# Kernel tuning notes

Hardware: AMD Instinct MI355X
Metric: run time of the kernel (lower is better)

Reference implementation:

```python
import jax, jax.numpy as jnp
import numpy as np

SIGMA = 5.0  # outlier threshold (LLM.int8()-style)


def setup_inputs() -> dict:
    key = jax.random.key(0)
    k1, k2 = jax.random.split(key)
    B, S, K, N = 4, 2048, 4096, 11008
    x = jax.random.normal(k1, (B, S, K), dtype=jnp.float32)
    weight = jax.random.normal(k2, (N, K), dtype=jnp.float32) * 0.02
    sigma = jnp.full((1,), SIGMA, dtype=jnp.float32)
    return {"x": x, "weight": weight, "sigma": sigma}


def reference(x, weight, sigma):
    # x: (..., K), weight: (N, K), sigma: (1,)
    N, K = weight.shape
    x2 = x.reshape(-1, K)  # (M, K)
    sig = sigma[0]

    # --- weight quantization (quant_weight, weight_only=False path) ---
    # note: torch's (1 << 8 - 1 - 1) == 1 << 6 == 64
    scale_col = jnp.max(jnp.abs(weight), axis=1) / 64.0          # (N,)
    q_weight = jnp.round(weight / scale_col[:, None])             # (N, K) int8-valued

    # --- FindOutliers: columns where any |x| > sigma ---
    col_mask = jnp.any(jnp.abs(x2) > sig, axis=0)                 # (K,) bool

    # ExtractOutliersAndSetToZeros
    x_out = jnp.where(col_mask[None, :], x2, 0.0)                 # outlier activations
    x_in = jnp.where(col_mask[None, :], 0.0, x2)                  # zeroed-out inputs

    # ExtractFP16weight: dequantized outlier weight columns; zero them in q_weight
    w_deq_out = q_weight * scale_col[:, None] * col_mask[None, :].astype(q_weight.dtype)
    q_w_in = jnp.where(col_mask[None, :], 0.0, q_weight)

    # fp16 outlier correction GEMM: (M, K) @ (K, N)
    outliers = x_out @ w_deq_out.T                                # (M, N)

    # per-row activation scale and int8 quantize
    x_scale = jnp.maximum(jnp.max(jnp.abs(x_in), axis=1) / 127.0, 1e-8)  # (M,)
    q_x = jnp.round(x_in / x_scale[:, None])                      # int8-valued

    # int8FusedDequantize: int8 GEMM + per-row/per-col dequant + outlier add
    y = (q_x @ q_w_in.T) * x_scale[:, None] * scale_col[None, :] + outliers
    return y.reshape(x.shape[:-1] + (N,))
```

## Files before the change

### kernel.cpp

```cpp
#include <hip/hip_runtime.h>
#include <hip/hip_bf16.h>
#include <stdint.h>

#define K_DIM 4096
#define BM 256
#define BN 256
#define BK 32
#define NT (K_DIM / BK)

typedef __bf16 bf16_t;
typedef __bf16 bf16x8 __attribute__((ext_vector_type(8)));
typedef __bf16 bf16x4 __attribute__((ext_vector_type(4)));
typedef float f32x4 __attribute__((ext_vector_type(4)));

__device__ inline void async16(const bf16_t* g, bf16_t* l) {
  __builtin_amdgcn_global_load_lds(
      (const __attribute__((address_space(1))) void*)g,
      (__attribute__((address_space(3))) void*)l, 16, 0, 0);
}


__device__ inline float wave_block_max(float v, float* red) {
  #pragma unroll
  for (int off = 32; off > 0; off >>= 1)
    v = fmaxf(v, __shfl_xor(v, off, 64));
  int lane = threadIdx.x & 63, wid = threadIdx.x >> 6;
  if (lane == 0) red[wid] = v;
  __syncthreads();
  return fmaxf(fmaxf(red[0], red[1]), fmaxf(red[2], red[3]));
}

__global__ __launch_bounds__(256) void colmask_kernel(
    const float* __restrict__ x, const float* __restrict__ sigma,
    int* __restrict__ mask, long total4) {
  float sig = sigma[0];
  long stride = (long)gridDim.x * blockDim.x;
  for (long i = (long)blockIdx.x * blockDim.x + threadIdx.x; i < total4;
       i += stride) {
    float4 v = ((const float4*)x)[i];
    int k = (int)((i * 4) & (K_DIM - 1));
    if (fabsf(v.x) > sig) mask[k + 0] = 1;
    if (fabsf(v.y) > sig) mask[k + 1] = 1;
    if (fabsf(v.z) > sig) mask[k + 2] = 1;
    if (fabsf(v.w) > sig) mask[k + 3] = 1;
  }
}

__global__ __launch_bounds__(256) void fused_w_kernel(
    const float* __restrict__ W, float* __restrict__ scale,
    bf16_t* __restrict__ Wq) {
  __shared__ float red[4];
  int n = blockIdx.x;
  const float4* row = (const float4*)(W + (size_t)n * K_DIM);
  float4 v[4];
  float amax = 0.f;
  #pragma unroll
  for (int j = 0; j < 4; j++) {
    v[j] = row[threadIdx.x + j * 256];
    amax = fmaxf(amax, fmaxf(fmaxf(fabsf(v[j].x), fabsf(v[j].y)),
                             fmaxf(fabsf(v[j].z), fabsf(v[j].w))));
  }
  float mx = wave_block_max(amax, red);
  float s = mx * (1.0f / 64.0f);
  if (threadIdx.x == 0) scale[n] = s;
  float is = (s > 0.f) ? 1.0f / s : 0.f;
  bf16_t* orow = Wq + (size_t)n * K_DIM;
  #pragma unroll
  for (int j = 0; j < 4; j++) {
    bf16x4 q;
    q[0] = (bf16_t)rintf(v[j].x * is);
    q[1] = (bf16_t)rintf(v[j].y * is);
    q[2] = (bf16_t)rintf(v[j].z * is);
    q[3] = (bf16_t)rintf(v[j].w * is);
    *(bf16x4*)(orow + (size_t)(threadIdx.x + j * 256) * 4) = q;
  }
}

__global__ __launch_bounds__(256) void fused_x_kernel(
    const float* __restrict__ x, const int* __restrict__ mask,
    float* __restrict__ xs, bf16_t* __restrict__ Aq) {
  __shared__ float red[4];
  int m = blockIdx.x;
  const float4* row = (const float4*)(x + (size_t)m * K_DIM);
  const int4* mk = (const int4*)mask;
  float4 v[4];
  int4 b[4];
  float amax = 0.f;
  #pragma unroll
  for (int j = 0; j < 4; j++) {
    v[j] = row[threadIdx.x + j * 256];
    b[j] = mk[threadIdx.x + j * 256];
    if (!b[j].x) amax = fmaxf(amax, fabsf(v[j].x));
    if (!b[j].y) amax = fmaxf(amax, fabsf(v[j].y));
    if (!b[j].z) amax = fmaxf(amax, fabsf(v[j].z));
    if (!b[j].w) amax = fmaxf(amax, fabsf(v[j].w));
  }
  float mx = wave_block_max(amax, red);
  float s = fmaxf(mx * (1.0f / 127.0f), 1e-8f);
  if (threadIdx.x == 0) xs[m] = s;
  float iv = 1.0f / s;
  bf16_t* orow = Aq + (size_t)m * K_DIM;
  #pragma unroll
  for (int j = 0; j < 4; j++) {
    float f0 = v[j].x * iv, f1 = v[j].y * iv, f2 = v[j].z * iv, f3 = v[j].w * iv;
    bf16x4 q;
    q[0] = (bf16_t)(b[j].x ? f0 : rintf(f0));
    q[1] = (bf16_t)(b[j].y ? f1 : rintf(f1));
    q[2] = (bf16_t)(b[j].z ? f2 : rintf(f2));
    q[3] = (bf16_t)(b[j].w ? f3 : rintf(f3));
    *(bf16x4*)(orow + (size_t)(threadIdx.x + j * 256) * 4) = q;
  }
}


__global__ __launch_bounds__(512, 2) void gemm_kernel(
    const bf16_t* __restrict__ A, const bf16_t* __restrict__ B,
    const float* __restrict__ xs, const float* __restrict__ sc,
    float* __restrict__ out, int M, int N) {
  __shared__ __align__(16) bf16_t lds[4 * 16384];

  const int tid  = threadIdx.x;
  const int lane = tid & 63;
  const int wave = tid >> 6;
  const int wmBase = (wave >> 2) * 128;
  const int wnBase = (wave & 3) * 64;
  const int l15  = lane & 15;
  const int quad = lane >> 4;
  const int swz8 = (quad ^ ((l15 >> 1) & 3)) * 8;

  const int ntn = N / BN;
  const int nwg = (M / BM) * ntn;
  int bid = blockIdx.x;
  int lid = (bid & 7) * (nwg >> 3) + (bid >> 3);
  const int g4 = ntn * 4;
  const int tm = (lid / g4) * 4 + (lid & 3);
  const int tn = (lid % g4) >> 2;
  const int bm = tm * BM;
  const int bn = tn * BN;

  const int srow = wave * 16 + (lane >> 2);
  const int scol = ((lane & 3) ^ ((lane >> 3) & 3)) * 8;
  const bf16_t* gA = A + (size_t)(bm + srow) * K_DIM + scol;
  const bf16_t* gB = B + (size_t)(bn + srow) * K_DIM + scol;
  bf16_t* ldsA = lds + wave * 512;
  bf16_t* ldsB = lds + 8192 + wave * 512;

  auto stageA = [&](int t) {
    const bf16_t* g = gA + (size_t)t * BK;
    bf16_t* d = ldsA + (t & 3) * 16384;
    async16(g, d);
    async16(g + (size_t)128 * K_DIM, d + 4096);
  };
  auto stageB = [&](int t) {
    const bf16_t* g = gB + (size_t)t * BK;
    bf16_t* d = ldsB + (t & 3) * 16384;
    async16(g, d);
    async16(g + (size_t)128 * K_DIM, d + 4096);
  };

  f32x4 acc[8][4];
  #pragma unroll
  for (int i = 0; i < 8; ++i)
    #pragma unroll
    for (int j = 0; j < 4; ++j)
      #pragma unroll
      for (int e = 0; e < 4; ++e) acc[i][j][e] = 0.f;

  stageA(0); stageB(0); stageA(1); stageB(1); stageA(2); stageB(2);
  asm volatile("s_waitcnt vmcnt(8)" ::: "memory");
  __builtin_amdgcn_s_barrier();

  for (int t = 0; t < NT; ++t) {
    const bf16_t* Asl = lds + (t & 3) * 16384;
    const bf16_t* Bsl = Asl + 8192;
    bf16x8 afA[4], bfr[4], afB[4];

    #pragma unroll
    for (int i = 0; i < 4; ++i)
      afA[i] = *(const bf16x8*)(Asl + (wmBase + i * 16 + l15) * 32 + swz8);
    #pragma unroll
    for (int j = 0; j < 4; ++j)
      bfr[j] = *(const bf16x8*)(Bsl + (wnBase + j * 16 + l15) * 32 + swz8);
    #pragma unroll
    for (int i = 0; i < 4; ++i)
      afB[i] = *(const bf16x8*)(Asl + (wmBase + 64 + i * 16 + l15) * 32 + swz8);

    if (t + 3 < NT) { stageA(t + 3); stageB(t + 3); }
    __builtin_amdgcn_sched_barrier(0);

    __builtin_amdgcn_s_setprio(1);
    #pragma unroll
    for (int i = 0; i < 4; ++i)
      #pragma unroll
      for (int j = 0; j < 4; ++j)
        acc[i][j] = __builtin_amdgcn_mfma_f32_16x16x32_bf16(afA[i], bfr[j],
                                                            acc[i][j], 0, 0, 0);
    __builtin_amdgcn_s_setprio(0);
    __builtin_amdgcn_sched_barrier(0);

    __builtin_amdgcn_s_setprio(1);
    #pragma unroll
    for (int i = 0; i < 4; ++i)
      #pragma unroll
      for (int j = 0; j < 4; ++j)
        acc[4 + i][j] = __builtin_amdgcn_mfma_f32_16x16x32_bf16(afB[i], bfr[j],
                                                                acc[4 + i][j], 0, 0, 0);
    __builtin_amdgcn_s_setprio(0);
    __builtin_amdgcn_sched_barrier(0);

    if (t + 1 < NT) {
      int rem = NT - 1 - t;
      if (rem >= 3)      asm volatile("s_waitcnt vmcnt(8)" ::: "memory");
      else if (rem == 2) asm volatile("s_waitcnt vmcnt(4)" ::: "memory");
      else               asm volatile("s_waitcnt vmcnt(0)" ::: "memory");
      __builtin_amdgcn_s_barrier();
    }
  }

  float scv[4];
  #pragma unroll
  for (int tj = 0; tj < 4; ++tj) scv[tj] = sc[bn + wnBase + tj * 16 + l15];
  #pragma unroll
  for (int mi = 0; mi < 8; ++mi) {
    #pragma unroll
    for (int i = 0; i < 4; ++i) {
      int row = bm + wmBase + mi * 16 + quad * 4 + i;
      float s_row = xs[row];
      float* orow = out + (size_t)row * N + bn + wnBase + l15;
      #pragma unroll
      for (int tj = 0; tj < 4; ++tj)
        orow[tj * 16] = acc[mi][tj][i] * s_row * scv[tj];
    }
  }
}


extern "C" void kernel_launch(void* const* d_in, const int* in_sizes, int n_in,
                              void* d_out, int out_size, void* d_ws, size_t ws_size,
                              hipStream_t stream) {
  const float* x = (const float*)d_in[0];
  const float* W = (const float*)d_in[1];
  const float* sigma = (const float*)d_in[2];
  float* out = (float*)d_out;

  const int K = K_DIM;
  const int M = in_sizes[0] / K;
  const int N = in_sizes[1] / K;

  char* ws = (char*)d_ws;
  size_t off = 0;
  auto alloc = [&](size_t bytes) -> void* {
    void* p = ws + off;
    off += (bytes + 255) & ~(size_t)255;
    return p;
  };
  float* scale_col = (float*)alloc((size_t)N * 4);
  int*   mask      = (int*)alloc((size_t)K * 4);
  float* xs        = (float*)alloc((size_t)M * 4);
  bf16_t* Wq       = (bf16_t*)alloc((size_t)N * K * 2);
  bf16_t* Aq       = (bf16_t*)alloc((size_t)M * K * 2);

  hipMemsetAsync(mask, 0, (size_t)K * sizeof(int), stream);

  long total4 = (long)M * K / 4;
  colmask_kernel<<<4096, 256, 0, stream>>>(x, sigma, mask, total4);

  fused_w_kernel<<<N, 256, 0, stream>>>(W, scale_col, Wq);
  fused_x_kernel<<<M, 256, 0, stream>>>(x, mask, xs, Aq);

  dim3 grid((M / BM) * (N / BN));
  gemm_kernel<<<grid, 512, 0, stream>>>(Aq, Wq, xs, scale_col, out, M, N);
}
```

Measured before the change: 1.202 ms.

## Software-pipeline LDS fragment loads with ping-pong registers and split global staging

Restructures the bf16 GEMM main loop so that each K-tile's second half of MFMAs overlaps with LDS reads of the next tile's A/B fragments. Ping-pong register sets alternate between tiles, and the A and B global-to-LDS async copies are issued in separate halves, with finer waitcnt and barrier placement. This is meant to hide LDS read latency and spread memory issue across the MFMA stream, at the cost of more registers (extra fragment sets) and more complex synchronization. The last four tiles keep a simpler epilogue loop.

```diff
diff --git a/kernel.cpp b/kernel.cpp
--- a/kernel.cpp
+++ b/kernel.cpp
@@ -166,56 +166,112 @@
       #pragma unroll
       for (int e = 0; e < 4; ++e) acc[i][j][e] = 0.f;
 
+  bf16x8 afA_p[4], bfr_p[4], afA_q[4], bfr_q[4], afB[4];
+
   stageA(0); stageB(0); stageA(1); stageB(1); stageA(2); stageB(2);
   asm volatile("s_waitcnt vmcnt(8)" ::: "memory");
   __builtin_amdgcn_s_barrier();
-
-  for (int t = 0; t < NT; ++t) {
-    const bf16_t* Asl = lds + (t & 3) * 16384;
+  {
+    const bf16_t* Asl = lds;
+    const bf16_t* Bsl = lds + 8192;
+    #pragma unroll
+    for (int i = 0; i < 4; ++i)
+      afA_p[i] = *(const bf16x8*)(Asl + (wmBase + i * 16 + l15) * 32 + swz8);
+    #pragma unroll
+    for (int j = 0; j < 4; ++j)
+      bfr_p[j] = *(const bf16x8*)(Bsl + (wnBase + j * 16 + l15) * 32 + swz8);
+  }
+
+#define HALF_TILE(U, AF_CUR, BF_CUR, AF_NXT, BF_NXT)                           \
+  {                                                                            \
+    const int u_ = (U);                                                        \
+    const bf16_t* Asl = lds + (u_ & 3) * 16384;                                \
+    const bf16_t* Nsl = lds + ((u_ + 1) & 3) * 16384;                          \
+                                                        \
+    __builtin_amdgcn_s_barrier();                                              \
+    _Pragma("unroll")                                                          \
+    for (int i = 0; i < 4; ++i)                                                \
+      afB[i] = *(const bf16x8*)(Asl + (wmBase + 64 + i * 16 + l15) * 32 + swz8);\
+    stageA(u_ + 3);                                                            \
+    asm volatile("s_waitcnt lgkmcnt(4)" ::: "memory");                         \
+    __builtin_amdgcn_sched_barrier(0);                                         \
+    __builtin_amdgcn_s_setprio(1);                                             \
+    _Pragma("unroll")                                                          \
+    for (int i = 0; i < 4; ++i)                                                \
+      _Pragma("unroll")                                                        \
+      for (int j = 0; j < 4; ++j)                                              \
+        acc[i][j] = __builtin_amdgcn_mfma_f32_16x16x32_bf16(                   \
+            AF_CUR[i], BF_CUR[j], acc[i][j], 0, 0, 0);                         \
+    __builtin_amdgcn_s_setprio(0);                                             \
+    __builtin_amdgcn_sched_barrier(0);                                         \
+                       \
+    asm volatile("s_waitcnt vmcnt(6)" ::: "memory");                           \
+    __builtin_amdgcn_s_barrier();                                              \
+    _Pragma("unroll")                                                          \
+    for (int i = 0; i < 4; ++i)                                                \
+      AF_NXT[i] = *(const bf16x8*)(Nsl + (wmBase + i * 16 + l15) * 32 + swz8); \
+    _Pragma("unroll")                                                          \
+    for (int j = 0; j < 4; ++j)                                                \
+      BF_NXT[j] = *(const bf16x8*)(Nsl + 8192 + (wnBase + j * 16 + l15) * 32 + swz8);\
+    stageB(u_ + 3);                                                            \
+    asm volatile("s_waitcnt lgkmcnt(8)" ::: "memory");                         \
+    __builtin_amdgcn_sched_barrier(0);                                         \
+    __builtin_amdgcn_s_setprio(1);                                             \
+    _Pragma("unroll")                                                          \
+    for (int i = 0; i < 4; ++i)                                                \
+      _Pragma("unroll")                                                        \
+      for (int j = 0; j < 4; ++j)                                              \
+        acc[4 + i][j] = __builtin_amdgcn_mfma_f32_16x16x32_bf16(               \
+            afB[i], BF_CUR[j], acc[4 + i][j], 0, 0, 0);                        \
+    __builtin_amdgcn_s_setprio(0);                                             \
+    __builtin_amdgcn_sched_barrier(0);                                         \
+  }
+
+  for (int t = 0; t + 5 < NT; t += 2) {
+    HALF_TILE(t,     afA_p, bfr_p, afA_q, bfr_q);
+    HALF_TILE(t + 1, afA_q, bfr_q, afA_p, bfr_p);
+  }
+
+  for (int u = NT - 4; u < NT; ++u) {
+    const bf16_t* Asl = lds + (u & 3) * 16384;
     const bf16_t* Bsl = Asl + 8192;
-    bf16x8 afA[4], bfr[4], afB[4];
-
-    #pragma unroll
-    for (int i = 0; i < 4; ++i)
-      afA[i] = *(const bf16x8*)(Asl + (wmBase + i * 16 + l15) * 32 + swz8);
+    __builtin_amdgcn_s_barrier();
+    bf16x8 a0[4], b0[4], a1[4];
+    #pragma unroll
+    for (int i = 0; i < 4; ++i)
+      a0[i] = *(const bf16x8*)(Asl + (wmBase + i * 16 + l15) * 32 + swz8);
     #pragma unroll
     for (int j = 0; j < 4; ++j)
-      bfr[j] = *(const bf16x8*)(Bsl + (wnBase + j * 16 + l15) * 32 + swz8);
-    #pragma unroll
-    for (int i = 0; i < 4; ++i)
-      afB[i] = *(const bf16x8*)(Asl + (wmBase + 64 + i * 16 + l15) * 32 + swz8);
-
-    if (t + 3 < NT) { stageA(t + 3); stageB(t + 3); }
+      b0[j] = *(const bf16x8*)(Bsl + (wnBase + j * 16 + l15) * 32 + swz8);
+    #pragma unroll
+    for (int i = 0; i < 4; ++i)
+      a1[i] = *(const bf16x8*)(Asl + (wmBase + 64 + i * 16 + l15) * 32 + swz8);
+    if (u + 3 < NT) { stageA(u + 3); stageB(u + 3); }
+    asm volatile("s_waitcnt lgkmcnt(0)" ::: "memory");
     __builtin_amdgcn_sched_barrier(0);
-
     __builtin_amdgcn_s_setprio(1);
     #pragma unroll
     for (int i = 0; i < 4; ++i)
       #pragma unroll
       for (int j = 0; j < 4; ++j)
-        acc[i][j] = __builtin_amdgcn_mfma_f32_16x16x32_bf16(afA[i], bfr[j],
+        acc[i][j] = __builtin_amdgcn_mfma_f32_16x16x32_bf16(a0[i], b0[j],
                                                             acc[i][j], 0, 0, 0);
-    __builtin_amdgcn_s_setprio(0);
-    __builtin_amdgcn_sched_barrier(0);
-
-    __builtin_amdgcn_s_setprio(1);
     #pragma unroll
     for (int i = 0; i < 4; ++i)
       #pragma unroll
       for (int j = 0; j < 4; ++j)
-        acc[4 + i][j] = __builtin_amdgcn_mfma_f32_16x16x32_bf16(afB[i], bfr[j],
+        acc[4 + i][j] = __builtin_amdgcn_mfma_f32_16x16x32_bf16(a1[i], b0[j],
                                                                 acc[4 + i][j], 0, 0, 0);
     __builtin_amdgcn_s_setprio(0);
     __builtin_amdgcn_sched_barrier(0);
-
-    if (t + 1 < NT) {
-      int rem = NT - 1 - t;
+    if (u + 1 < NT) {
+      int rem = NT - 1 - u;
       if (rem >= 3)      asm volatile("s_waitcnt vmcnt(8)" ::: "memory");
       else if (rem == 2) asm volatile("s_waitcnt vmcnt(4)" ::: "memory");
       else               asm volatile("s_waitcnt vmcnt(0)" ::: "memory");
-      __builtin_amdgcn_s_barrier();
     }
   }
+#undef HALF_TILE
 
   float scv[4];
   #pragma unroll
```

New measurement: 1.154 ms. 4.0% less time.
